# Kernel optimization log

Hardware: AMD Instinct MI355X
Metric: run time of the kernel (lower is better)

Reference implementation:

```python
import jax, jax.numpy as jnp
import numpy as np
from jax import lax

NB_HEADS = 8
SR_RATIO = 4
LN_EPS = 1e-6


def layer_norm(x, g, b):
    mu = jnp.mean(x, axis=-1, keepdims=True)
    var = jnp.mean(jnp.square(x - mu), axis=-1, keepdims=True)
    return (x - mu) * lax.rsqrt(var + LN_EPS) * g + b


def setup_inputs() -> dict:
    key = jax.random.key(0)
    ks = jax.random.split(key, 6)
    B, H, W, C = 16, 64, 64, 256
    N = H * W
    s = 0.02
    return {
        "x": jax.random.normal(ks[0], (B, N, C), jnp.float32),
        "q_w": jax.random.normal(ks[1], (C, C), jnp.float32) * s,
        "q_b": jnp.zeros((C,), jnp.float32),
        "kv_w": jax.random.normal(ks[2], (C, 2 * C), jnp.float32) * s,
        "kv_b": jnp.zeros((2 * C,), jnp.float32),
        "sr_w": jax.random.normal(ks[3], (SR_RATIO, SR_RATIO, C, C), jnp.float32) * s,
        "sr_b": jnp.zeros((C,), jnp.float32),
        "norm_g": jnp.ones((C,), jnp.float32),
        "norm_b": jnp.zeros((C,), jnp.float32),
        "proj_w": jax.random.normal(ks[4], (C, C), jnp.float32) * s,
        "proj_b": jnp.zeros((C,), jnp.float32),
        "grid_h": H,
        "grid_w": W,
    }


def reference(x, q_w, q_b, kv_w, kv_b, sr_w, sr_b, norm_g, norm_b, proj_w, proj_b, grid_h, grid_w):
    B, N, C = x.shape
    hd = C // NB_HEADS
    scale = hd ** (-0.5)

    # query projection -> [B, nh, N, hd]
    q = (x @ q_w + q_b).reshape(B, N, NB_HEADS, hd).transpose(0, 2, 1, 3)

    # spatial reduction: conv stride=kernel=sr_ratio on NHWC grid
    xg = x.reshape(B, grid_h, grid_w, C)
    xs = lax.conv_general_dilated(
        xg, sr_w, window_strides=(SR_RATIO, SR_RATIO), padding="VALID",
        dimension_numbers=("NHWC", "HWIO", "NHWC")) + sr_b
    M = (grid_h // SR_RATIO) * (grid_w // SR_RATIO)
    xs = layer_norm(xs.reshape(B, M, C), norm_g, norm_b)

    # key/value projection -> [B, nh, M, hd] each
    kv = (xs @ kv_w + kv_b).reshape(B, M, 2, NB_HEADS, hd).transpose(2, 0, 3, 1, 4)
    k, v = kv[0], kv[1]

    attn = jax.nn.softmax(scale * jnp.einsum("bhnd,bhmd->bhnm", q, k), axis=-1)
    out = jnp.einsum("bhnm,bhmd->bhnd", attn, v)  # [B, nh, N, hd]
    out = out.transpose(0, 2, 1, 3).reshape(B, N, C)
    return out @ proj_w + proj_b
```

## Files before the change

### kernel.cpp

```cpp
#include <hip/hip_runtime.h>
#include <math.h>

#define B_   16
#define CC   256
#define NN   4096
#define MM   256
#define NH   8
#define HD   32
#define QSCALE (0.17677669529663687f * 1.4426950408889634f)

typedef float fx4 __attribute__((ext_vector_type(4)));
typedef short sx4 __attribute__((ext_vector_type(4)));
typedef short sx8 __attribute__((ext_vector_type(8)));

__device__ inline short f2bf(float f) {
  unsigned u = __builtin_bit_cast(unsigned, f);
  u += 0x7FFFu + ((u >> 16) & 1u);
  return (short)(u >> 16);
}
__device__ inline float bf2f(short s) {
  unsigned u = ((unsigned)(unsigned short)s) << 16;
  return __builtin_bit_cast(float, u);
}
__device__ inline float fexp2(float x) {
#if __has_builtin(__builtin_amdgcn_exp2f)
  return __builtin_amdgcn_exp2f(x);
#else
  return exp2f(x);
#endif
}
__device__ inline float frcp(float x) {
#if __has_builtin(__builtin_amdgcn_rcpf)
  return __builtin_amdgcn_rcpf(x);
#else
  return 1.0f / x;
#endif
}

__global__ __launch_bounds__(256) void wsplit_kernel(
    const float* __restrict__ W, short* __restrict__ Th, short* __restrict__ Tl,
    int K, int N)
{
  __shared__ float Tile[64][65];
  const int t = threadIdx.x;
  const int k0 = blockIdx.y << 6, n0 = blockIdx.x << 6;
#pragma unroll
  for (int i = 0; i < 4; ++i) {
    int idx = t + (i << 8);
    int k = idx >> 4, n4 = (idx & 15) << 2;
    float4 v = *(const float4*)&W[(size_t)(k0 + k) * N + n0 + n4];
    Tile[k][n4 + 0] = v.x; Tile[k][n4 + 1] = v.y;
    Tile[k][n4 + 2] = v.z; Tile[k][n4 + 3] = v.w;
  }
  __syncthreads();
#pragma unroll
  for (int i = 0; i < 4; ++i) {
    int idx = t + (i << 8);
    int n = idx >> 4, k4 = (idx & 15) << 2;
    sx4 h, lo;
#pragma unroll
    for (int j = 0; j < 4; ++j) {
      float v = Tile[k4 + j][n];
      short hh = f2bf(v);
      h[j] = hh;
      lo[j] = f2bf(v - bf2f(hh));
    }
    *(sx4*)&Th[(size_t)(n0 + n) * K + k0 + k4] = h;
    *(sx4*)&Tl[(size_t)(n0 + n) * K + k0 + k4] = lo;
  }
}

template<int AMODE, int EPI>
__global__ __launch_bounds__(256) void gemm_split_kernel(
    const void* __restrict__ Av, const short* __restrict__ Alo,
    const short* __restrict__ Bth, const short* __restrict__ Btl,
    const float* __restrict__ bias,
    float* __restrict__ C, short* __restrict__ kout, short* __restrict__ vout,
    int M, int N, int K)
{
  __shared__ short Ah[64][40], Al[64][40], Bh[64][40], Bl[64][40];
  const int t = threadIdx.x;
  const int bm = blockIdx.y << 6, bn = blockIdx.x << 6;
  const int ar = t >> 2, ak = (t & 3) << 3;
  const int bc = t >> 2, bk = (t & 3) << 3;
  const float* Af  = (const float*)Av;
  const short* Ahg = (const short*)Av;

  int sp_base = 0;
  if (AMODE == 1) {
    int gr = bm + ar;
    int b = gr >> 8, mm2 = gr & 255;
    int oh = mm2 >> 4, ow = mm2 & 15;
    sp_base = b * 4096 + oh * 256 + ow * 4;
  }
  const size_t brow = (size_t)(bn + bc) * K;

  const int KS = K / gridDim.z;
  const int kbeg = blockIdx.z * KS, kend = kbeg + KS;

  float4 pa0, pa1; sx8 pah, pal, pbh, pbl;
  auto LOADG = [&](int k0) {
    int k = k0 + ak;
    if constexpr (AMODE == 2) {
      int row = bm + ar;
      int b = row >> 12, n = row & 4095;
      size_t idx = ((size_t)b << 20) + ((size_t)(k >> 5) << 17) + ((size_t)n << 5) + (k & 31);
      pah = *(const sx8*)&Ahg[idx];
      pal = *(const sx8*)&Alo[idx];
    } else {
      const float* ap;
      if constexpr (AMODE == 1) {
        int pos = k >> 8, ci = k & 255;
        ap = &Af[(size_t)(sp_base + ((pos >> 2) << 6) + (pos & 3)) * 256 + ci];
      } else {
        ap = &Af[(size_t)(bm + ar) * K + k];
      }
      pa0 = *(const float4*)ap;
      pa1 = *(const float4*)(ap + 4);
    }
    pbh = *(const sx8*)&Bth[brow + k0 + bk];
    pbl = *(const sx8*)&Btl[brow + k0 + bk];
  };

  const int w = t >> 6, l = t & 63, g = l >> 4, c = l & 15;
  const int wr = w >> 1, wc = w & 1;
  const int ra0 = (wr << 5) + c, ra1 = ra0 + 16;
  const int cb0 = (wc << 5) + c, cb1 = cb0 + 16;
  const int g8 = g << 3;

  fx4 acc00 = {0.f,0.f,0.f,0.f}, acc01 = acc00, acc10 = acc00, acc11 = acc00;

  LOADG(kbeg);
  for (int k0 = kbeg; k0 < kend; k0 += 32) {
    if constexpr (AMODE == 2) {
      *(sx8*)&Ah[ar][ak] = pah;
      *(sx8*)&Al[ar][ak] = pal;
    } else {
      sx4 AH0, AL0, AH1, AL1;
      AH0[0]=f2bf(pa0.x); AL0[0]=f2bf(pa0.x-bf2f(AH0[0]));
      AH0[1]=f2bf(pa0.y); AL0[1]=f2bf(pa0.y-bf2f(AH0[1]));
      AH0[2]=f2bf(pa0.z); AL0[2]=f2bf(pa0.z-bf2f(AH0[2]));
      AH0[3]=f2bf(pa0.w); AL0[3]=f2bf(pa0.w-bf2f(AH0[3]));
      AH1[0]=f2bf(pa1.x); AL1[0]=f2bf(pa1.x-bf2f(AH1[0]));
      AH1[1]=f2bf(pa1.y); AL1[1]=f2bf(pa1.y-bf2f(AH1[1]));
      AH1[2]=f2bf(pa1.z); AL1[2]=f2bf(pa1.z-bf2f(AH1[2]));
      AH1[3]=f2bf(pa1.w); AL1[3]=f2bf(pa1.w-bf2f(AH1[3]));
      *(sx4*)&Ah[ar][ak]     = AH0;  *(sx4*)&Ah[ar][ak + 4] = AH1;
      *(sx4*)&Al[ar][ak]     = AL0;  *(sx4*)&Al[ar][ak + 4] = AL1;
    }
    *(sx8*)&Bh[bc][bk] = pbh;      *(sx8*)&Bl[bc][bk] = pbl;
    __syncthreads();
    if (k0 + 32 < kend) LOADG(k0 + 32);

    sx8 a0h = *(const sx8*)&Ah[ra0][g8];
    sx8 a0l = *(const sx8*)&Al[ra0][g8];
    sx8 a1h = *(const sx8*)&Ah[ra1][g8];
    sx8 a1l = *(const sx8*)&Al[ra1][g8];
    sx8 b0h = *(const sx8*)&Bh[cb0][g8];
    sx8 b0l = *(const sx8*)&Bl[cb0][g8];
    sx8 b1h = *(const sx8*)&Bh[cb1][g8];
    sx8 b1l = *(const sx8*)&Bl[cb1][g8];

    acc00 = __builtin_amdgcn_mfma_f32_16x16x32_bf16(a0h, b0h, acc00, 0, 0, 0);
    acc01 = __builtin_amdgcn_mfma_f32_16x16x32_bf16(a0h, b1h, acc01, 0, 0, 0);
    acc10 = __builtin_amdgcn_mfma_f32_16x16x32_bf16(a1h, b0h, acc10, 0, 0, 0);
    acc11 = __builtin_amdgcn_mfma_f32_16x16x32_bf16(a1h, b1h, acc11, 0, 0, 0);
    acc00 = __builtin_amdgcn_mfma_f32_16x16x32_bf16(a0l, b0h, acc00, 0, 0, 0);
    acc01 = __builtin_amdgcn_mfma_f32_16x16x32_bf16(a0l, b1h, acc01, 0, 0, 0);
    acc10 = __builtin_amdgcn_mfma_f32_16x16x32_bf16(a1l, b0h, acc10, 0, 0, 0);
    acc11 = __builtin_amdgcn_mfma_f32_16x16x32_bf16(a1l, b1h, acc11, 0, 0, 0);
    acc00 = __builtin_amdgcn_mfma_f32_16x16x32_bf16(a0h, b0l, acc00, 0, 0, 0);
    acc01 = __builtin_amdgcn_mfma_f32_16x16x32_bf16(a0h, b1l, acc01, 0, 0, 0);
    acc10 = __builtin_amdgcn_mfma_f32_16x16x32_bf16(a1h, b0l, acc10, 0, 0, 0);
    acc11 = __builtin_amdgcn_mfma_f32_16x16x32_bf16(a1h, b1l, acc11, 0, 0, 0);
    __syncthreads();
  }

  const int col0 = bn + (wc << 5);
  const int row0 = bm + (wr << 5) + (g << 2);
  if constexpr (EPI == 0) {
    const float b0 = bias[col0 + c], b1 = bias[col0 + 16 + c];
#pragma unroll
    for (int i = 0; i < 4; ++i) {
      C[(size_t)(row0 + i) * N + col0 + c]           = acc00[i] + b0;
      C[(size_t)(row0 + i) * N + col0 + 16 + c]      = acc01[i] + b1;
      C[(size_t)(row0 + 16 + i) * N + col0 + c]      = acc10[i] + b0;
      C[(size_t)(row0 + 16 + i) * N + col0 + 16 + c] = acc11[i] + b1;
    }
  } else if constexpr (EPI == 1) {
    float* Cz = C + (size_t)blockIdx.z * M * N;
#pragma unroll
    for (int i = 0; i < 4; ++i) {
      Cz[(size_t)(row0 + i) * N + col0 + c]           = acc00[i];
      Cz[(size_t)(row0 + i) * N + col0 + 16 + c]      = acc01[i];
      Cz[(size_t)(row0 + 16 + i) * N + col0 + c]      = acc10[i];
      Cz[(size_t)(row0 + 16 + i) * N + col0 + 16 + c] = acc11[i];
    }
  } else if constexpr (EPI == 2) {
    const float b0 = bias[col0 + c], b1 = bias[col0 + 16 + c];
    auto emit = [&](int row, int n, float v) {
      int b = row >> 8, m = row & 255;
      short* dst = (n < 256) ? kout : vout;
      int nn = n & 255;
      int h = nn >> 5, d = nn & 31;
      dst[(size_t)(((b << 3) + h) * 256 + m) * 32 + d] = f2bf(v);
    };
#pragma unroll
    for (int i = 0; i < 4; ++i) {
      emit(row0 + i,      col0 + c,      acc00[i] + b0);
      emit(row0 + i,      col0 + 16 + c, acc01[i] + b1);
      emit(row0 + 16 + i, col0 + c,      acc10[i] + b0);
      emit(row0 + 16 + i, col0 + 16 + c, acc11[i] + b1);
    }
  } else {
    const float b0 = bias[col0 + c], b1 = bias[col0 + 16 + c];
    auto emitq = [&](int row, int n, float v) {
      int b = row >> 12, nn = row & 4095;
      int h = n >> 5, d = n & 31;
      kout[(size_t)(((b << 3) + h) * 4096 + nn) * 32 + d] = f2bf(v * QSCALE);
    };
#pragma unroll
    for (int i = 0; i < 4; ++i) {
      emitq(row0 + i,      col0 + c,      acc00[i] + b0);
      emitq(row0 + i,      col0 + 16 + c, acc01[i] + b1);
      emitq(row0 + 16 + i, col0 + c,      acc10[i] + b0);
      emitq(row0 + 16 + i, col0 + 16 + c, acc11[i] + b1);
    }
  }
}

__global__ __launch_bounds__(256) void ln_reduce_kernel(
    const float* __restrict__ parts, const float* __restrict__ bias,
    const float* __restrict__ g, const float* __restrict__ bta,
    float* __restrict__ xs)
{
  const int row = blockIdx.x, t = threadIdx.x;
  const size_t MN = (size_t)4096 * 256;
  const size_t off = (size_t)row * CC + t;
  float v = parts[off] + parts[MN + off] + parts[2*MN + off] + parts[3*MN + off] + bias[t];
  float s = v, s2 = v * v;
#pragma unroll
  for (int offs = 32; offs; offs >>= 1) {
    s  += __shfl_xor(s,  offs, 64);
    s2 += __shfl_xor(s2, offs, 64);
  }
  __shared__ float red[8];
  const int w = t >> 6, lane = t & 63;
  if (lane == 0) { red[w] = s; red[4 + w] = s2; }
  __syncthreads();
  float ts  = red[0] + red[1] + red[2] + red[3];
  float ts2 = red[4] + red[5] + red[6] + red[7];
  float mu  = ts * (1.0f / 256.0f);
  float var = ts2 * (1.0f / 256.0f) - mu * mu;
  float o = (v - mu) * rsqrtf(var + 1e-6f) * g[t] + bta[t];
  xs[off] = o;
}

__global__ __launch_bounds__(256, 3) void attn_mfma3_kernel(
    short* __restrict__ qob, short* __restrict__ olo,
    const short* __restrict__ kbf, const short* __restrict__ vbf)
{
  __shared__ short Vt[32 * 264];
  __shared__ short Ps[4 * 16 * 264];

  const int tid = threadIdx.x;
  const int bid = blockIdx.x;
  const int nt = bid & 63, h = (bid >> 6) & 7, b = bid >> 9;
  const int n0 = nt << 6;
  const int bh = (b << 3) + h;
  const short* kb = kbf + (size_t)bh * 256 * 32;
  const short* vb = vbf + (size_t)bh * 256 * 32;

  {
    sx8 v0 = *(const sx8*)&vb[tid * 32 + 0];
    sx8 v1 = *(const sx8*)&vb[tid * 32 + 8];
    sx8 v2 = *(const sx8*)&vb[tid * 32 + 16];
    sx8 v3 = *(const sx8*)&vb[tid * 32 + 24];
#pragma unroll
    for (int e = 0; e < 8; ++e) {
      Vt[(e)      * 264 + tid] = v0[e];
      Vt[(8 + e)  * 264 + tid] = v1[e];
      Vt[(16 + e) * 264 + tid] = v2[e];
      Vt[(24 + e) * 264 + tid] = v3[e];
    }
  }

  const int w = tid >> 6, l = tid & 63;
  const int g = l >> 4, c = l & 15;

  sx8 aq = *(const sx8*)&qob[((size_t)bh * 4096 + n0 + w * 16 + c) * 32 + (g << 3)];

  fx4 acc[16];
#pragma unroll
  for (int j = 0; j < 16; ++j) {
    sx8 bk = *(const sx8*)&kb[(j * 16 + c) * 32 + (g << 3)];
    fx4 z = {0.f, 0.f, 0.f, 0.f};
    acc[j] = __builtin_amdgcn_mfma_f32_16x16x32_bf16(aq, bk, z, 0, 0, 0);
  }

  float mx[4], sm[4];
#pragma unroll
  for (int i = 0; i < 4; ++i) {
    float m0 = acc[0][i];
#pragma unroll
    for (int j = 1; j < 16; ++j) m0 = fmaxf(m0, acc[j][i]);
    m0 = fmaxf(m0, __shfl_xor(m0, 1, 64));
    m0 = fmaxf(m0, __shfl_xor(m0, 2, 64));
    m0 = fmaxf(m0, __shfl_xor(m0, 4, 64));
    m0 = fmaxf(m0, __shfl_xor(m0, 8, 64));
    mx[i] = m0;
  }
#pragma unroll
  for (int i = 0; i < 4; ++i) {
    float s0 = 0.f;
#pragma unroll
    for (int j = 0; j < 16; ++j) {
      float p = fexp2(acc[j][i] - mx[i]);
      acc[j][i] = p; s0 += p;
    }
    s0 += __shfl_xor(s0, 1, 64);
    s0 += __shfl_xor(s0, 2, 64);
    s0 += __shfl_xor(s0, 4, 64);
    s0 += __shfl_xor(s0, 8, 64);
    sm[i] = s0;
  }

  const int pbase = (w << 4) * 264;
#pragma unroll
  for (int j = 0; j < 16; ++j) {
#pragma unroll
    for (int i = 0; i < 4; ++i)
      Ps[pbase + ((g << 2) + i) * 264 + (j << 4) + c] = f2bf(acc[j][i]);
  }

  __syncthreads();

  fx4 o0 = {0.f,0.f,0.f,0.f}, o1 = {0.f,0.f,0.f,0.f};
#pragma unroll
  for (int s = 0; s < 8; ++s) {
    sx8 ap  = *(const sx8*)&Ps[pbase + c * 264 + (s << 5) + (g << 3)];
    sx8 bv0 = *(const sx8*)&Vt[(c)      * 264 + (s << 5) + (g << 3)];
    sx8 bv1 = *(const sx8*)&Vt[(16 + c) * 264 + (s << 5) + (g << 3)];
    o0 = __builtin_amdgcn_mfma_f32_16x16x32_bf16(ap, bv0, o0, 0, 0, 0);
    o1 = __builtin_amdgcn_mfma_f32_16x16x32_bf16(ap, bv1, o1, 0, 0, 0);
  }

#pragma unroll
  for (int i = 0; i < 4; ++i) {
    float inv = frcp(sm[i]);
    int n = n0 + w * 16 + (g << 2) + i;
    size_t base = ((size_t)bh * 4096 + n) * 32;
    float v0 = o0[i] * inv, v1 = o1[i] * inv;
    short h0 = f2bf(v0), h1 = f2bf(v1);
    qob[base + c]      = h0;  olo[base + c]      = f2bf(v0 - bf2f(h0));
    qob[base + 16 + c] = h1;  olo[base + 16 + c] = f2bf(v1 - bf2f(h1));
  }
}

extern "C" void kernel_launch(void* const* d_in, const int* in_sizes, int n_in,
                              void* d_out, int out_size, void* d_ws, size_t ws_size,
                              hipStream_t stream) {
  const float* x      = (const float*)d_in[0];
  const float* q_w    = (const float*)d_in[1];
  const float* q_b    = (const float*)d_in[2];
  const float* kv_w   = (const float*)d_in[3];
  const float* kv_b   = (const float*)d_in[4];
  const float* sr_w   = (const float*)d_in[5];
  const float* sr_b   = (const float*)d_in[6];
  const float* norm_g = (const float*)d_in[7];
  const float* norm_b = (const float*)d_in[8];
  const float* proj_w = (const float*)d_in[9];
  const float* proj_b = (const float*)d_in[10];
  float* out = (float*)d_out;

  float* xsbuf = (float*)d_ws;
  short* qbf   = (short*)(xsbuf + 1048576);
  float* partf = (float*)qbf;
  short* olo   = qbf + 16777216;
  short* kbf   = olo + 16777216;
  short* vbf   = kbf + 2097152;
  short* qwt_h  = vbf + 2097152;
  short* qwt_l  = qwt_h + 65536;
  short* kvwt_h = qwt_l + 65536;
  short* kvwt_l = kvwt_h + 131072;
  short* pwt_h  = kvwt_l + 131072;
  short* pwt_l  = pwt_h + 65536;
  short* swt_h  = pwt_l + 65536;
  short* swt_l  = swt_h + 1048576;

  dim3 blk(256);

  wsplit_kernel<<<dim3(CC/64, CC/64), blk, 0, stream>>>(q_w, qwt_h, qwt_l, CC, CC);
  wsplit_kernel<<<dim3(2*CC/64, CC/64), blk, 0, stream>>>(kv_w, kvwt_h, kvwt_l, CC, 2*CC);
  wsplit_kernel<<<dim3(CC/64, CC/64), blk, 0, stream>>>(proj_w, pwt_h, pwt_l, CC, CC);
  wsplit_kernel<<<dim3(CC/64, 4096/64), blk, 0, stream>>>(sr_w, swt_h, swt_l, 4096, CC);

  gemm_split_kernel<1,1><<<dim3(CC/64, (B_*MM)/64, 4), blk, 0, stream>>>(
      x, nullptr, swt_h, swt_l, sr_b, partf, nullptr, nullptr, B_*MM, CC, 4096);

  ln_reduce_kernel<<<B_ * MM, blk, 0, stream>>>(partf, sr_b, norm_g, norm_b, xsbuf);

  gemm_split_kernel<0,2><<<dim3((2*CC)/64, (B_*MM)/64, 1), blk, 0, stream>>>(
      xsbuf, nullptr, kvwt_h, kvwt_l, kv_b, nullptr, kbf, vbf, B_*MM, 2*CC, CC);

  gemm_split_kernel<0,3><<<dim3(CC/64, (B_*NN)/64, 1), blk, 0, stream>>>(
      x, nullptr, qwt_h, qwt_l, q_b, nullptr, qbf, nullptr, B_*NN, CC, CC);

  attn_mfma3_kernel<<<B_ * NH * (NN / 64), blk, 0, stream>>>(qbf, olo, kbf, vbf);

  gemm_split_kernel<2,0><<<dim3(CC/64, (B_*NN)/64, 1), blk, 0, stream>>>(
      qbf, olo, pwt_h, pwt_l, proj_b, out, nullptr, nullptr, B_*NN, CC, CC);
}
```

Baseline: 237.4 us.

## Reuse Q-GEMM bf16 split of x for SR conv and pack P stores

The Q projection GEMM now runs first and, from its column-0 blocks, writes the hi/lo bf16 split of x to scratch buffers. The spatial-reduction conv GEMM then reads these pre-split bf16 values instead of reloading fp32 x and converting again. This halves the bytes read for the conv and removes redundant conversion work, at the cost of extra writes and reusing the output buffer as scratch. In attention, the key order is permuted so each lane's P values are contiguous, letting them be packed with v_cvt_pk_bf16_f32 and stored as 128-bit vectors instead of scalar 16-bit stores.

New measurement: 274.6 us. 15.7% more time.

```diff
diff --git a/kernel.cpp b/kernel.cpp
--- a/kernel.cpp
+++ b/kernel.cpp
@@ -22,6 +22,11 @@
   unsigned u = ((unsigned)(unsigned short)s) << 16;
   return __builtin_bit_cast(float, u);
 }
+__device__ inline unsigned cvtpk_bf16(float a, float b) {
+  unsigned r;
+  asm("v_cvt_pk_bf16_f32 %0, %1, %2" : "=v"(r) : "v"(a), "v"(b));
+  return r;
+}
 __device__ inline float fexp2(float x) {
 #if __has_builtin(__builtin_amdgcn_exp2f)
   return __builtin_amdgcn_exp2f(x);
@@ -76,6 +81,7 @@
     const short* __restrict__ Bth, const short* __restrict__ Btl,
     const float* __restrict__ bias,
     float* __restrict__ C, short* __restrict__ kout, short* __restrict__ vout,
+    short* __restrict__ xh, short* __restrict__ xl,
     int M, int N, int K)
 {
   __shared__ short Ah[64][40], Al[64][40], Bh[64][40], Bl[64][40];
@@ -87,7 +93,7 @@
   const short* Ahg = (const short*)Av;
 
   int sp_base = 0;
-  if (AMODE == 1) {
+  if (AMODE == 4) {
     int gr = bm + ar;
     int b = gr >> 8, mm2 = gr & 255;
     int oh = mm2 >> 4, ow = mm2 & 15;
@@ -101,20 +107,22 @@
   float4 pa0, pa1; sx8 pah, pal, pbh, pbl;
   auto LOADG = [&](int k0) {
     int k = k0 + ak;
-    if constexpr (AMODE == 2) {
-      int row = bm + ar;
-      int b = row >> 12, n = row & 4095;
-      size_t idx = ((size_t)b << 20) + ((size_t)(k >> 5) << 17) + ((size_t)n << 5) + (k & 31);
+    if constexpr (AMODE >= 2) {
+      size_t idx;
+      if constexpr (AMODE == 2) {
+        int row = bm + ar;
+        int b = row >> 12, n = row & 4095;
+        idx = ((size_t)b << 20) + ((size_t)(k >> 5) << 17) + ((size_t)n << 5) + (k & 31);
+      } else if constexpr (AMODE == 3) {
+        idx = (size_t)(bm + ar) * K + k;
+      } else {
+        int pos = k >> 8, ci = k & 255;
+        idx = (size_t)(sp_base + ((pos >> 2) << 6) + (pos & 3)) * 256 + ci;
+      }
       pah = *(const sx8*)&Ahg[idx];
       pal = *(const sx8*)&Alo[idx];
     } else {
-      const float* ap;
-      if constexpr (AMODE == 1) {
-        int pos = k >> 8, ci = k & 255;
-        ap = &Af[(size_t)(sp_base + ((pos >> 2) << 6) + (pos & 3)) * 256 + ci];
-      } else {
-        ap = &Af[(size_t)(bm + ar) * K + k];
-      }
+      const float* ap = &Af[(size_t)(bm + ar) * K + k];
       pa0 = *(const float4*)ap;
       pa1 = *(const float4*)(ap + 4);
     }
@@ -132,7 +140,7 @@
 
   LOADG(kbeg);
   for (int k0 = kbeg; k0 < kend; k0 += 32) {
-    if constexpr (AMODE == 2) {
+    if constexpr (AMODE >= 2) {
       *(sx8*)&Ah[ar][ak] = pah;
       *(sx8*)&Al[ar][ak] = pal;
     } else {
@@ -147,6 +155,15 @@
       AH1[3]=f2bf(pa1.w); AL1[3]=f2bf(pa1.w-bf2f(AH1[3]));
       *(sx4*)&Ah[ar][ak]     = AH0;  *(sx4*)&Ah[ar][ak + 4] = AH1;
       *(sx4*)&Al[ar][ak]     = AL0;  *(sx4*)&Al[ar][ak + 4] = AL1;
+      if constexpr (EPI == 3) {
+        if (blockIdx.x == 0) {
+          sx8 h8 = { AH0[0],AH0[1],AH0[2],AH0[3], AH1[0],AH1[1],AH1[2],AH1[3] };
+          sx8 l8 = { AL0[0],AL0[1],AL0[2],AL0[3], AL1[0],AL1[1],AL1[2],AL1[3] };
+          size_t xi = (size_t)(bm + ar) * 256 + k0 + ak;
+          *(sx8*)&xh[xi] = h8;
+          *(sx8*)&xl[xi] = l8;
+        }
+      }
     }
     *(sx8*)&Bh[bc][bk] = pbh;      *(sx8*)&Bl[bc][bk] = pbl;
     __syncthreads();
@@ -256,7 +273,7 @@
   xs[off] = o;
 }
 
-__global__ __launch_bounds__(256, 3) void attn_mfma3_kernel(
+__global__ __launch_bounds__(256, 3) void attn_mfma4_kernel(
     short* __restrict__ qob, short* __restrict__ olo,
     const short* __restrict__ kbf, const short* __restrict__ vbf)
 {
@@ -268,14 +285,15 @@
   const int nt = bid & 63, h = (bid >> 6) & 7, b = bid >> 9;
   const int n0 = nt << 6;
   const int bh = (b << 3) + h;
-  const short* kb = kbf + (size_t)bh * 256 * 32;
-  const short* vb = vbf + (size_t)bh * 256 * 32;
+  const short* kb = kbf + (size_t)bh * 8192;
+  const short* vb = vbf + (size_t)bh * 8192;
 
   {
-    sx8 v0 = *(const sx8*)&vb[tid * 32 + 0];
-    sx8 v1 = *(const sx8*)&vb[tid * 32 + 8];
-    sx8 v2 = *(const sx8*)&vb[tid * 32 + 16];
-    sx8 v3 = *(const sx8*)&vb[tid * 32 + 24];
+    const int msrc = ((tid & 15) << 4) | (tid >> 4);
+    sx8 v0 = *(const sx8*)&vb[msrc * 32 + 0];
+    sx8 v1 = *(const sx8*)&vb[msrc * 32 + 8];
+    sx8 v2 = *(const sx8*)&vb[msrc * 32 + 16];
+    sx8 v3 = *(const sx8*)&vb[msrc * 32 + 24];
 #pragma unroll
     for (int e = 0; e < 8; ++e) {
       Vt[(e)      * 264 + tid] = v0[e];
@@ -327,10 +345,20 @@
 
   const int pbase = (w << 4) * 264;
 #pragma unroll
-  for (int j = 0; j < 16; ++j) {
-#pragma unroll
-    for (int i = 0; i < 4; ++i)
-      Ps[pbase + ((g << 2) + i) * 264 + (j << 4) + c] = f2bf(acc[j][i]);
+  for (int i = 0; i < 4; ++i) {
+    unsigned p0 = cvtpk_bf16(acc[0][i],  acc[1][i]);
+    unsigned p1 = cvtpk_bf16(acc[2][i],  acc[3][i]);
+    unsigned p2 = cvtpk_bf16(acc[4][i],  acc[5][i]);
+    unsigned p3 = cvtpk_bf16(acc[6][i],  acc[7][i]);
+    unsigned p4 = cvtpk_bf16(acc[8][i],  acc[9][i]);
+    unsigned p5 = cvtpk_bf16(acc[10][i], acc[11][i]);
+    unsigned p6 = cvtpk_bf16(acc[12][i], acc[13][i]);
+    unsigned p7 = cvtpk_bf16(acc[14][i], acc[15][i]);
+    unsigned* dst = (unsigned*)&Ps[pbase + ((g << 2) + i) * 264 + (c << 4)];
+    uint4 lo4; lo4.x = p0; lo4.y = p1; lo4.z = p2; lo4.w = p3;
+    uint4 hi4; hi4.x = p4; hi4.y = p5; hi4.z = p6; hi4.w = p7;
+    *(uint4*)dst       = lo4;
+    *(uint4*)(dst + 4) = hi4;
   }
 
   __syncthreads();
@@ -375,7 +403,6 @@
 
   float* xsbuf = (float*)d_ws;
   short* qbf   = (short*)(xsbuf + 1048576);
-  float* partf = (float*)qbf;
   short* olo   = qbf + 16777216;
   short* kbf   = olo + 16777216;
   short* vbf   = kbf + 2097152;
@@ -387,6 +414,9 @@
   short* pwt_l  = pwt_h + 65536;
   short* swt_h  = pwt_l + 65536;
   short* swt_l  = swt_h + 1048576;
+  float* partf = out;
+  short* xh    = olo;
+  short* xl    = (short*)(out + 4194304);
 
   dim3 blk(256);
 
@@ -395,19 +425,19 @@
   wsplit_kernel<<<dim3(CC/64, CC/64), blk, 0, stream>>>(proj_w, pwt_h, pwt_l, CC, CC);
   wsplit_kernel<<<dim3(CC/64, 4096/64), blk, 0, stream>>>(sr_w, swt_h, swt_l, 4096, CC);
 
-  gemm_split_kernel<1,1><<<dim3(CC/64, (B_*MM)/64, 4), blk, 0, stream>>>(
-      x, nullptr, swt_h, swt_l, sr_b, partf, nullptr, nullptr, B_*MM, CC, 4096);
+  gemm_split_kernel<0,3><<<dim3(CC/64, (B_*NN)/64, 1), blk, 0, stream>>>(
+      x, nullptr, qwt_h, qwt_l, q_b, nullptr, qbf, nullptr, xh, xl, B_*NN, CC, CC);
+
+  gemm_split_kernel<4,1><<<dim3(CC/64, (B_*MM)/64, 4), blk, 0, stream>>>(
+      xh, xl, swt_h, swt_l, sr_b, partf, nullptr, nullptr, nullptr, nullptr, B_*MM, CC, 4096);
 
   ln_reduce_kernel<<<B_ * MM, blk, 0, stream>>>(partf, sr_b, norm_g, norm_b, xsbuf);
 
   gemm_split_kernel<0,2><<<dim3((2*CC)/64, (B_*MM)/64, 1), blk, 0, stream>>>(
-      xsbuf, nullptr, kvwt_h, kvwt_l, kv_b, nullptr, kbf, vbf, B_*MM, 2*CC, CC);
-
-  gemm_split_kernel<0,3><<<dim3(CC/64, (B_*NN)/64, 1), blk, 0, stream>>>(
-      x, nullptr, qwt_h, qwt_l, q_b, nullptr, qbf, nullptr, B_*NN, CC, CC);
-
-  attn_mfma3_kernel<<<B_ * NH * (NN / 64), blk, 0, stream>>>(qbf, olo, kbf, vbf);
+      xsbuf, nullptr, kvwt_h, kvwt_l, kv_b, nullptr, kbf, vbf, nullptr, nullptr, B_*MM, 2*CC, CC);
+
+  attn_mfma4_kernel<<<B_ * NH * (NN / 64), blk, 0, stream>>>(qbf, olo, kbf, vbf);
 
   gemm_split_kernel<2,0><<<dim3(CC/64, (B_*NN)/64, 1), blk, 0, stream>>>(
-      qbf, olo, pwt_h, pwt_l, proj_b, out, nullptr, nullptr, B_*NN, CC, CC);
-}
+      qbf, olo, pwt_h, pwt_l, proj_b, out, nullptr, nullptr, nullptr, nullptr, B_*NN, CC, CC);
+}
```
